# Optimization experiments

Measured on AMD Instinct MI355X. Metric: run time of the kernel, lower is better.

The kernel has to match this reference:

```python
import jax, jax.numpy as jnp
import numpy as np

UNITS = 256
FEAT = 256
NUM_BLOCKS = 4  # start_gru + 2 middle blocks + end_gru
BATCH, T = 128, 384


def _gru_layer(x, kernel, rkernel, bias, return_sequences):
    """Keras GRU (reset_after=True, tanh/sigmoid), zero initial state.
    x: [B,T,D]; kernel: [D,3U]; rkernel: [U,3U]; bias: [2,3U] (input, recurrent).
    Gate order z, r, h as in Keras.
    """
    u = rkernel.shape[0]
    # Precompute input projections for all timesteps (one big GEMM)
    xp = jnp.einsum('btd,dg->btg', x, kernel) + bias[0]  # [B,T,3U]

    def step(h, xt):
        rh = h @ rkernel + bias[1]                 # [B,3U]
        mz, mr, mh = jnp.split(xt, 3, axis=-1)
        rz, rr, rhh = jnp.split(rh, 3, axis=-1)
        z = jax.nn.sigmoid(mz + rz)
        r = jax.nn.sigmoid(mr + rr)
        hh = jnp.tanh(mh + r * rhh)                # reset_after: r applied after recurrent matmul
        h_new = z * h + (1.0 - z) * hh
        return h_new, h_new

    h0 = jnp.zeros((x.shape[0], u), dtype=x.dtype)
    hT, hs = jax.lax.scan(step, h0, jnp.swapaxes(xp, 0, 1))  # scan over time
    return jnp.swapaxes(hs, 0, 1) if return_sequences else hT


def setup_inputs() -> dict:
    key = jax.random.key(0)
    ks = jax.random.split(key, 8)
    s_in = 1.0 / np.sqrt(FEAT)
    s_u = 1.0 / np.sqrt(UNITS)
    x = jax.random.normal(ks[0], (BATCH, T, FEAT), dtype=jnp.float32)
    # first layer params
    k0 = jax.random.normal(ks[1], (FEAT, 3 * UNITS), dtype=jnp.float32) * s_in
    rk0 = jax.random.normal(ks[2], (UNITS, 3 * UNITS), dtype=jnp.float32) * s_u
    b0 = jnp.zeros((2, 3 * UNITS), dtype=jnp.float32)
    # remaining NUM_BLOCKS-1 layers, stacked along leading axis
    L = NUM_BLOCKS - 1
    kern = jax.random.normal(ks[3], (L, UNITS, 3 * UNITS), dtype=jnp.float32) * s_u
    rkern = jax.random.normal(ks[4], (L, UNITS, 3 * UNITS), dtype=jnp.float32) * s_u
    bias = jnp.zeros((L, 2, 3 * UNITS), dtype=jnp.float32)
    return {"x": x, "k0": k0, "rk0": rk0, "b0": b0,
            "kern": kern, "rkern": rkern, "bias": bias}


def reference(x, k0, rk0, b0, kern, rkern, bias):
    # start_gru: return_sequences=True
    h = _gru_layer(x, k0, rk0, b0, return_sequences=True)
    L = kern.shape[0]
    # middle blocks return_sequences=True, last (end_gru) returns final state only
    for i in range(L):
        last = (i == L - 1)
        h = _gru_layer(h, kern[i], rkern[i], bias[i], return_sequences=not last)
    return h  # [B, UNITS]
```

## Files before the change

kernel.cpp:

```cpp
#include <hip/hip_runtime.h>
#include <hip/hip_fp16.h>


#define LAYERS 4
#define TSTEPS 384
#define NCH    8
#define WPL    (48 * 16 * 64 * 8)
#define TILE_STRIDE (16 * 64 * 8)
#define RING   16
#define SLOT_ULL (16 * 128)
#define GRP_ULL  (RING * SLOT_ULL)

typedef _Float16 half8 __attribute__((ext_vector_type(8)));
typedef float    f32x4 __attribute__((ext_vector_type(4)));
typedef unsigned uint4v __attribute__((ext_vector_type(4)));
typedef unsigned long long ull;

#define WP_OFF   0
#define BP_OFF   (LAYERS * WPL * 2)
#define FLAG_OFF (BP_OFF + LAYERS * 1024 * 4)
#define FLAG_BYTES 4096
#define HBUF_OFF (4 * 1024 * 1024)

__global__ void repack_kernel(const float* __restrict__ k0, const float* __restrict__ rk0,
                              const float* __restrict__ b0, const float* __restrict__ kern,
                              const float* __restrict__ rkern, const float* __restrict__ bias,
                              _Float16* __restrict__ Wp, float* __restrict__ Bp)
{
    int idx = blockIdx.x * 256 + threadIdx.x;
    const int total_w = LAYERS * WPL;
    if (idx < total_w) {
        int l = idx / WPL;
        int r = idx - l * WPL;
        int j    = r & 7;
        int lane = (r >> 3) & 63;
        int kt   = (r >> 9) & 15;
        int tile = r >> 13;
        int n = tile * 16 + (lane & 15);
        int k = kt * 32 + (lane >> 4) * 8 + j;
        float v;
        if (l == 0) {
            v = (k < 256) ? k0[(size_t)k * 768 + n] : rk0[(size_t)(k - 256) * 768 + n];
        } else {
            const float* kk = kern  + (size_t)(l - 1) * 256 * 768;
            const float* rk = rkern + (size_t)(l - 1) * 256 * 768;
            v = (k < 256) ? kk[(size_t)k * 768 + n] : rk[(size_t)(k - 256) * 768 + n];
        }
        Wp[idx] = (_Float16)v;
    } else {
        int ib = idx - total_w;
        if (ib < LAYERS * 1024) {
            int l = ib >> 10;
            int i = ib & 1023;
            const float* bs = (l == 0) ? b0 : (bias + (size_t)(l - 1) * 2 * 768);
            float v;
            if (i < 512)      v = bs[i] + bs[768 + i];
            else if (i < 768) v = bs[512 + (i - 512)];
            else              v = bs[768 + 512 + (i - 768)];
            Bp[l * 1024 + i] = v;
        }
    }
}

__launch_bounds__(384, 1)
__global__ void gru_kernel(const float* __restrict__ x,
                           const _Float16* __restrict__ Wp,
                           const float* __restrict__ Bp,
                           ull* __restrict__ hbuf,
                           unsigned int* __restrict__ flags,
                           float* __restrict__ out)
{
    __shared__ _Float16 Af[2][16 * 512];
    __shared__ float    Sc[8][16][17];

    const int tid  = threadIdx.x;
    const int lane = tid & 63;
    const int w    = tid >> 6;
    const int lo16 = lane & 15;
    const int q    = lane >> 4;

    const int s = blockIdx.x & 7;
    const int c = (blockIdx.x >> 3) & 7;
    const int l = blockIdx.x >> 6;
    const int b0row = c * 16;

    const int tile = (w >> 1) * 16 + 2 * s + (w & 1);
    half8 bfrag[16];
    {
        const _Float16* wb = Wp + (size_t)l * WPL + (size_t)tile * TILE_STRIDE;
#pragma unroll
        for (int kt = 0; kt < 16; ++kt)
            bfrag[kt] = *(const half8*)(wb + ((size_t)kt * 64 + lane) * 8);
    }

    const int grow = tid >> 4;
    const int g16  = tid & 15;
    const int gup  = g16 * 2;
    const int ktx  = g16 >> 1;
    const int qq   = (g16 & 1) * 2;
    const int xoff0 = ((ktx * 64) + qq * 16 + grow) * 8;
    const int xoff1 = ((ktx * 64) + (qq + 1) * 16 + grow) * 8;
    const int hoff0 = (((8 + ktx) * 64) + qq * 16 + grow) * 8;
    const int hoff1 = (((8 + ktx) * 64) + (qq + 1) * 16 + grow) * 8;

    float bz[2] = {0,0}, br[2] = {0,0}, bi[2] = {0,0}, bh[2] = {0,0};
    float hprev[2] = {0.f, 0.f};
    if (tid < 256) {
        const float* bp = Bp + l * 1024;
        int ug = s * 32 + gup;
        bz[0] = bp[ug];       bz[1] = bp[ug + 1];
        br[0] = bp[256 + ug]; br[1] = bp[256 + ug + 1];
        bi[0] = bp[512 + ug]; bi[1] = bp[512 + ug + 1];
        bh[0] = bp[768 + ug]; bh[1] = bp[768 + ug + 1];
    }

    unsigned int* fl_own_g = flags + (l * NCH + c) * 16;
    unsigned int* fl_dn_g  = flags + ((l < 3 ? l + 1 : 0) * NCH + c) * 16;
    unsigned int* my_flag  = fl_own_g + s;

    ull*       hb_own = hbuf + (size_t)(l * NCH + c) * GRP_ULL;
    const ull* hb_up  = hbuf + (size_t)((l > 0 ? l - 1 : 0) * NCH + c) * GRP_ULL;

    auto wait_group = [&](const unsigned int* base, unsigned need) {
        for (;;) {
            unsigned v = 0xFFFFFFFFu;
            if (lane < 8)
                v = __hip_atomic_load(base + lane, __ATOMIC_RELAXED,
                                      __HIP_MEMORY_SCOPE_SYSTEM);
            if (__all((int)(v >= need))) return;
            __builtin_amdgcn_s_sleep(1);
        }
    };

    auto stage_x = [&](int t, _Float16* An) {
        if (l == 0) {
            const float* sp = x + ((size_t)(b0row + grow) * TSTEPS + t) * 256 + gup * 8;
            f32x4 a0 = *(const f32x4*)sp,      a1 = *(const f32x4*)(sp + 4);
            f32x4 a2 = *(const f32x4*)(sp + 8), a3 = *(const f32x4*)(sp + 12);
            half8 h0, h1;
            h0[0]=(_Float16)a0[0]; h0[1]=(_Float16)a0[1]; h0[2]=(_Float16)a0[2]; h0[3]=(_Float16)a0[3];
            h0[4]=(_Float16)a1[0]; h0[5]=(_Float16)a1[1]; h0[6]=(_Float16)a1[2]; h0[7]=(_Float16)a1[3];
            h1[0]=(_Float16)a2[0]; h1[1]=(_Float16)a2[1]; h1[2]=(_Float16)a2[2]; h1[3]=(_Float16)a2[3];
            h1[4]=(_Float16)a3[0]; h1[5]=(_Float16)a3[1]; h1[6]=(_Float16)a3[2]; h1[7]=(_Float16)a3[3];
            *(half8*)(An + xoff0) = h0;
            *(half8*)(An + xoff1) = h1;
        } else {
            const ull* spx = hb_up + (size_t)(t & (RING - 1)) * SLOT_ULL + grow * 128 + g16 * 8;
            const unsigned tg = (unsigned)(t + 1);
            ull vx[8];
#pragma unroll
            for (int j = 0; j < 8; ++j)
                vx[j] = __hip_atomic_load(spx + j, __ATOMIC_RELAXED, __HIP_MEMORY_SCOPE_SYSTEM);
            for (;;) {
                bool ok = true;
#pragma unroll
                for (int j = 0; j < 8; ++j)
                    if ((unsigned)(vx[j] >> 32) != tg) {
                        vx[j] = __hip_atomic_load(spx + j, __ATOMIC_RELAXED, __HIP_MEMORY_SCOPE_SYSTEM);
                        ok = false;
                    }
                if (ok) break;
                __builtin_amdgcn_s_sleep(1);
            }
            uint4v w0, w1;
            w0[0]=(unsigned)vx[0]; w0[1]=(unsigned)vx[1]; w0[2]=(unsigned)vx[2]; w0[3]=(unsigned)vx[3];
            w1[0]=(unsigned)vx[4]; w1[1]=(unsigned)vx[5]; w1[2]=(unsigned)vx[6]; w1[3]=(unsigned)vx[7];
            *(uint4v*)(An + xoff0) = w0;
            *(uint4v*)(An + xoff1) = w1;
        }
    };

    if (tid < 256) {
        stage_x(0, Af[0]);
        uint4v z = {0u, 0u, 0u, 0u};
        *(uint4v*)(Af[0] + hoff0) = z;
        *(uint4v*)(Af[0] + hoff1) = z;
    }

    ull vh[8];

    for (int t = 0; t < TSTEPS; ++t) {
        _Float16* A  = Af[t & 1];
        _Float16* An = Af[(t + 1) & 1];

        if (t > 0 && tid < 256) {
            const ull* sph = hb_own + (size_t)((t - 1) & (RING - 1)) * SLOT_ULL + grow * 128 + g16 * 8;
            const unsigned tg = (unsigned)t;
            for (;;) {
                bool ok = true;
#pragma unroll
                for (int j = 0; j < 8; ++j)
                    if ((unsigned)(vh[j] >> 32) != tg) {
                        vh[j] = __hip_atomic_load(sph + j, __ATOMIC_RELAXED, __HIP_MEMORY_SCOPE_SYSTEM);
                        ok = false;
                    }
                if (ok) break;
            }
            uint4v w0, w1;
            w0[0]=(unsigned)vh[0]; w0[1]=(unsigned)vh[1]; w0[2]=(unsigned)vh[2]; w0[3]=(unsigned)vh[3];
            w1[0]=(unsigned)vh[4]; w1[1]=(unsigned)vh[5]; w1[2]=(unsigned)vh[6]; w1[3]=(unsigned)vh[7];
            *(uint4v*)(A + hoff0) = w0;
            *(uint4v*)(A + hoff1) = w1;
        }
        __syncthreads();

        f32x4 acc0 = {0,0,0,0}, acc1 = {0,0,0,0};
#pragma unroll
        for (int kt = 0; kt < 16; ++kt) {
            half8 a = *(const half8*)(A + ((kt * 64) + lane) * 8);
            if (w < 4 || kt < 8)
                acc0 = __builtin_amdgcn_mfma_f32_16x16x32_f16(a, bfrag[kt], acc0, 0, 0, 0);
            else
                acc1 = __builtin_amdgcn_mfma_f32_16x16x32_f16(a, bfrag[kt], acc1, 0, 0, 0);
        }
#pragma unroll
        for (int r = 0; r < 4; ++r) Sc[w][q * 4 + r][lo16] = acc0[r];
        if (w >= 4) {
#pragma unroll
            for (int r = 0; r < 4; ++r) Sc[w + 2][q * 4 + r][lo16] = acc1[r];
        }
        __syncthreads();

        if (l < 3 && t >= RING) wait_group(fl_dn_g, (unsigned)(t - RING + 1));

        if (tid < 256) {
            float hn[2];
#pragma unroll
            for (int j = 0; j < 2; ++j) {
                int u   = gup + j;
                int ut  = u >> 4;
                int col = u & 15;
                float zp = Sc[ut][grow][col]     + bz[j];
                float rp = Sc[2 + ut][grow][col] + br[j];
                float ip = Sc[4 + ut][grow][col] + bi[j];
                float hp = Sc[6 + ut][grow][col] + bh[j];
                float z  = 1.f / (1.f + __expf(-zp));
                float rr = 1.f / (1.f + __expf(-rp));
                float pre = ip + rr * hp;
                float e  = __expf(2.f * pre);
                float th = 1.f - 2.f / (e + 1.f);
                hn[j] = z * hprev[j] + (1.f - z) * th;
                hprev[j] = hn[j];
            }
            union { _Float16 h[2]; unsigned u32; } pk;
            pk.h[0] = (_Float16)hn[0];
            pk.h[1] = (_Float16)hn[1];
            ull word = ((ull)(unsigned)(t + 1) << 32) | (ull)pk.u32;
            __hip_atomic_store(hb_own + (size_t)(t & (RING - 1)) * SLOT_ULL + grow * 128 + s * 16 + g16,
                               word, __ATOMIC_RELAXED, __HIP_MEMORY_SCOPE_SYSTEM);
            if (l == 3 && t == TSTEPS - 1) {
                float* op = out + (size_t)(b0row + grow) * 256 + s * 32 + gup;
                op[0] = hn[0];
                op[1] = hn[1];
            }
        }

        if (t + 1 < TSTEPS && tid < 256) {
            stage_x(t + 1, An);
            const ull* sph = hb_own + (size_t)(t & (RING - 1)) * SLOT_ULL + grow * 128 + g16 * 8;
#pragma unroll
            for (int j = 0; j < 8; ++j)
                vh[j] = __hip_atomic_load(sph + j, __ATOMIC_RELAXED, __HIP_MEMORY_SCOPE_SYSTEM);
        }
        __syncthreads();

        if (tid == 0)
            __hip_atomic_store(my_flag, (unsigned)(t + 1),
                               __ATOMIC_RELAXED, __HIP_MEMORY_SCOPE_SYSTEM);
    }
}

extern "C" void kernel_launch(void* const* d_in, const int* in_sizes, int n_in,
                              void* d_out, int out_size, void* d_ws, size_t ws_size,
                              hipStream_t stream)
{
    const float* x     = (const float*)d_in[0];
    const float* k0    = (const float*)d_in[1];
    const float* rk0   = (const float*)d_in[2];
    const float* b0    = (const float*)d_in[3];
    const float* kern  = (const float*)d_in[4];
    const float* rkern = (const float*)d_in[5];
    const float* bias  = (const float*)d_in[6];
    float* out = (float*)d_out;

    char* ws = (char*)d_ws;
    _Float16*     Wp    = (_Float16*)(ws + WP_OFF);
    float*        Bp    = (float*)(ws + BP_OFF);
    unsigned int* flags = (unsigned int*)(ws + FLAG_OFF);
    ull*          hbuf  = (ull*)(ws + HBUF_OFF);

    hipMemsetAsync(flags, 0, FLAG_BYTES, stream);

    const int total = LAYERS * WPL + LAYERS * 1024;
    repack_kernel<<<(total + 255) / 256, 256, 0, stream>>>(k0, rk0, b0, kern, rkern, bias, Wp, Bp);

    gru_kernel<<<LAYERS * NCH * 8, 384, 0, stream>>>(x, Wp, Bp, hbuf, flags, out);
}
```

Before: 1.714 ms.

## Split GRU into recurrent and input-projection blocks with per-call epoch tags

Moves each layer's input projection out of the recurrent loop and onto separate producer blocks. Two of them per layer and chunk handle alternating timesteps and hand results to the recurrent block through a ring buffer in global memory. Each recurrent block now holds the full 256x768 recurrent weight slice for 16 batch rows in registers and LDS, so the hidden state is exchanged within one workgroup instead of across 8 blocks through global memory. A per-launch epoch counter makes the hbuf tags unique across calls, avoiding stale matches. The cost is more global traffic for the projections, stored as fp16 for z/r, and more complex flag protocols.

```diff
diff --git a/kernel.cpp b/kernel.cpp
--- a/kernel.cpp
+++ b/kernel.cpp
@@ -1,33 +1,41 @@
 #include <hip/hip_runtime.h>
-#include <hip/hip_fp16.h>
 
 
 #define LAYERS 4
 #define TSTEPS 384
-#define NCH    8
-#define WPL    (48 * 16 * 64 * 8)
+#define WPL (48 * 16 * 64 * 8)
 #define TILE_STRIDE (16 * 64 * 8)
-#define RING   16
-#define SLOT_ULL (16 * 128)
-#define GRP_ULL  (RING * SLOT_ULL)
+#define RING_H 16
+#define RING_X 8
+#define HSLOT 2048ull
+#define HGRP (RING_H * HSLOT)
+#define XSLOT_B 32768ull
+#define XGRP_B (RING_X * XSLOT_B)
 
 typedef _Float16 half8 __attribute__((ext_vector_type(8)));
 typedef float    f32x4 __attribute__((ext_vector_type(4)));
-typedef unsigned uint4v __attribute__((ext_vector_type(4)));
 typedef unsigned long long ull;
 
 #define WP_OFF   0
 #define BP_OFF   (LAYERS * WPL * 2)
 #define FLAG_OFF (BP_OFF + LAYERS * 1024 * 4)
 #define FLAG_BYTES 4096
-#define HBUF_OFF (4 * 1024 * 1024)
+#define EP_OFF   (FLAG_OFF + FLAG_BYTES)
+#define HBUF_OFF (4ull << 20)
+#define XP_OFF   (HBUF_OFF + 24ull * HGRP * 8ull)
+
+#define AL __ATOMIC_RELAXED
+#define SS __HIP_MEMORY_SCOPE_SYSTEM
+#define MFMA __builtin_amdgcn_mfma_f32_16x16x32_f16
 
 __global__ void repack_kernel(const float* __restrict__ k0, const float* __restrict__ rk0,
                               const float* __restrict__ b0, const float* __restrict__ kern,
                               const float* __restrict__ rkern, const float* __restrict__ bias,
-                              _Float16* __restrict__ Wp, float* __restrict__ Bp)
+                              _Float16* __restrict__ Wp, float* __restrict__ Bp,
+                              unsigned* __restrict__ ep)
 {
     int idx = blockIdx.x * 256 + threadIdx.x;
+    if (idx == 0) ep[0] = ep[0] + 1u;
     const int total_w = LAYERS * WPL;
     if (idx < total_w) {
         int l = idx / WPL;
@@ -62,211 +70,311 @@
     }
 }
 
-__launch_bounds__(384, 1)
+__launch_bounds__(512, 2)
 __global__ void gru_kernel(const float* __restrict__ x,
                            const _Float16* __restrict__ Wp,
                            const float* __restrict__ Bp,
                            ull* __restrict__ hbuf,
-                           unsigned int* __restrict__ flags,
+                           unsigned* __restrict__ flags,
+                           const unsigned* __restrict__ ep,
+                           char* __restrict__ xpb,
                            float* __restrict__ out)
 {
-    __shared__ _Float16 Af[2][16 * 512];
-    __shared__ float    Sc[8][16][17];
+    __shared__ _Float16 Af[2][8][65][8];
+    __shared__ _Float16 Bl[8][8][64][8];
 
     const int tid  = threadIdx.x;
     const int lane = tid & 63;
     const int w    = tid >> 6;
     const int lo16 = lane & 15;
     const int q    = lane >> 4;
-
-    const int s = blockIdx.x & 7;
-    const int c = (blockIdx.x >> 3) & 7;
-    const int l = blockIdx.x >> 6;
+    const unsigned tagbase = ep[0] * 1024u;
+
+    const bool isrec = (blockIdx.x < 32);
+    int l, c, par = 0;
+    if (isrec) { l = blockIdx.x >> 3; c = blockIdx.x & 7; }
+    else { int p = blockIdx.x - 32; l = p >> 4; c = (p >> 1) & 7; par = p & 1; }
     const int b0row = c * 16;
 
-    const int tile = (w >> 1) * 16 + 2 * s + (w & 1);
-    half8 bfrag[16];
+    half8 bf0[8], bf1[8], bf2[8], bf3[8], bf4[8];
     {
-        const _Float16* wb = Wp + (size_t)l * WPL + (size_t)tile * TILE_STRIDE;
-#pragma unroll
-        for (int kt = 0; kt < 16; ++kt)
-            bfrag[kt] = *(const half8*)(wb + ((size_t)kt * 64 + lane) * 8);
+        const _Float16* wb = Wp + (size_t)l * WPL;
+        const int kb = isrec ? 8 : 0;
+        const int t0 = 2*w, t1 = 2*w+1, t2 = 16+2*w, t3 = 17+2*w, t4 = 32+2*w, t5 = 33+2*w;
+#pragma unroll
+        for (int kt = 0; kt < 8; ++kt) {
+            size_t o = (size_t)((kb + kt) * 64 + lane) * 8;
+            bf0[kt] = *(const half8*)(wb + (size_t)t0 * TILE_STRIDE + o);
+            bf1[kt] = *(const half8*)(wb + (size_t)t1 * TILE_STRIDE + o);
+            bf2[kt] = *(const half8*)(wb + (size_t)t2 * TILE_STRIDE + o);
+            bf3[kt] = *(const half8*)(wb + (size_t)t3 * TILE_STRIDE + o);
+            bf4[kt] = *(const half8*)(wb + (size_t)t4 * TILE_STRIDE + o);
+            *(half8*)&Bl[w][kt][lane][0] = *(const half8*)(wb + (size_t)t5 * TILE_STRIDE + o);
+        }
     }
 
-    const int grow = tid >> 4;
-    const int g16  = tid & 15;
-    const int gup  = g16 * 2;
-    const int ktx  = g16 >> 1;
-    const int qq   = (g16 & 1) * 2;
-    const int xoff0 = ((ktx * 64) + qq * 16 + grow) * 8;
-    const int xoff1 = ((ktx * 64) + (qq + 1) * 16 + grow) * 8;
-    const int hoff0 = (((8 + ktx) * 64) + qq * 16 + grow) * 8;
-    const int hoff1 = (((8 + ktx) * 64) + (qq + 1) * 16 + grow) * 8;
-
-    float bz[2] = {0,0}, br[2] = {0,0}, bi[2] = {0,0}, bh[2] = {0,0};
-    float hprev[2] = {0.f, 0.f};
-    if (tid < 256) {
-        const float* bp = Bp + l * 1024;
-        int ug = s * 32 + gup;
-        bz[0] = bp[ug];       bz[1] = bp[ug + 1];
-        br[0] = bp[256 + ug]; br[1] = bp[256 + ug + 1];
-        bi[0] = bp[512 + ug]; bi[1] = bp[512 + ug + 1];
-        bh[0] = bp[768 + ug]; bh[1] = bp[768 + ug + 1];
-    }
-
-    unsigned int* fl_own_g = flags + (l * NCH + c) * 16;
-    unsigned int* fl_dn_g  = flags + ((l < 3 ? l + 1 : 0) * NCH + c) * 16;
-    unsigned int* my_flag  = fl_own_g + s;
-
-    ull*       hb_own = hbuf + (size_t)(l * NCH + c) * GRP_ULL;
-    const ull* hb_up  = hbuf + (size_t)((l > 0 ? l - 1 : 0) * NCH + c) * GRP_ULL;
-
-    auto wait_group = [&](const unsigned int* base, unsigned need) {
-        for (;;) {
-            unsigned v = 0xFFFFFFFFu;
-            if (lane < 8)
-                v = __hip_atomic_load(base + lane, __ATOMIC_RELAXED,
-                                      __HIP_MEMORY_SCOPE_SYSTEM);
-            if (__all((int)(v >= need))) return;
+    if (isrec) {
+        ull* hb_own = hbuf + (size_t)(l * 8 + c) * HGRP;
+        char* xg = xpb + (size_t)(l * 8 + c) * XGRP_B;
+        unsigned* rprog = flags + 128 + (l * 8 + c);
+        const ull* xf_pair = (const ull*)(flags + (l * 8 + c) * 2);
+        const ull* pp_pair = (const ull*)(flags + ((l < 3 ? l + 1 : l) * 8 + c) * 2);
+
+        float bh0, bh1;
+        {
+            const float* bp = Bp + l * 1024;
+            bh0 = bp[768 + 32 * w + lo16];
+            bh1 = bp[768 + 32 * w + 16 + lo16];
+        }
+
+        if (tid < 520) {
+            half8 z8 = {};
+            *(half8*)&Af[0][tid / 65][tid % 65][0] = z8;
+        }
+
+        float hprev[2][4] = {{0,0,0,0},{0,0,0,0}};
+        ull xzr[4], xip[4];
+        ull xfv, ppv = 0;
+
+        xfv = __hip_atomic_load(xf_pair, AL, SS);
+        while ((unsigned)(xfv & 0xffffffffu) < 1u) {
             __builtin_amdgcn_s_sleep(1);
-        }
-    };
-
-    auto stage_x = [&](int t, _Float16* An) {
-        if (l == 0) {
-            const float* sp = x + ((size_t)(b0row + grow) * TSTEPS + t) * 256 + gup * 8;
-            f32x4 a0 = *(const f32x4*)sp,      a1 = *(const f32x4*)(sp + 4);
-            f32x4 a2 = *(const f32x4*)(sp + 8), a3 = *(const f32x4*)(sp + 12);
-            half8 h0, h1;
-            h0[0]=(_Float16)a0[0]; h0[1]=(_Float16)a0[1]; h0[2]=(_Float16)a0[2]; h0[3]=(_Float16)a0[3];
-            h0[4]=(_Float16)a1[0]; h0[5]=(_Float16)a1[1]; h0[6]=(_Float16)a1[2]; h0[7]=(_Float16)a1[3];
-            h1[0]=(_Float16)a2[0]; h1[1]=(_Float16)a2[1]; h1[2]=(_Float16)a2[2]; h1[3]=(_Float16)a2[3];
-            h1[4]=(_Float16)a3[0]; h1[5]=(_Float16)a3[1]; h1[6]=(_Float16)a3[2]; h1[7]=(_Float16)a3[3];
-            *(half8*)(An + xoff0) = h0;
-            *(half8*)(An + xoff1) = h1;
-        } else {
-            const ull* spx = hb_up + (size_t)(t & (RING - 1)) * SLOT_ULL + grow * 128 + g16 * 8;
-            const unsigned tg = (unsigned)(t + 1);
-            ull vx[8];
-#pragma unroll
-            for (int j = 0; j < 8; ++j)
-                vx[j] = __hip_atomic_load(spx + j, __ATOMIC_RELAXED, __HIP_MEMORY_SCOPE_SYSTEM);
-            for (;;) {
-                bool ok = true;
-#pragma unroll
-                for (int j = 0; j < 8; ++j)
-                    if ((unsigned)(vx[j] >> 32) != tg) {
-                        vx[j] = __hip_atomic_load(spx + j, __ATOMIC_RELAXED, __HIP_MEMORY_SCOPE_SYSTEM);
-                        ok = false;
+            xfv = __hip_atomic_load(xf_pair, AL, SS);
+        }
+        {
+            const ull* xz = (const ull*)xg;
+            const ull* xi = (const ull*)(xg + 16384);
+#pragma unroll
+            for (int g = 0; g < 4; ++g)
+                xzr[g] = __hip_atomic_load(xz + (w * 4 + g) * 64 + lane, AL, SS);
+#pragma unroll
+            for (int gi = 0; gi < 2; ++gi)
+#pragma unroll
+                for (int h2 = 0; h2 < 2; ++h2)
+                    xip[gi * 2 + h2] = __hip_atomic_load(xi + ((w * 2 + gi) * 64 + lane) * 2 + h2, AL, SS);
+        }
+        xfv = __hip_atomic_load(xf_pair, AL, SS);
+        if (l < 3) ppv = __hip_atomic_load(pp_pair, AL, SS);
+        __syncthreads();
+
+        for (int t = 0; t < TSTEPS; ++t) {
+            const int cb = t & 1, nb = cb ^ 1;
+
+            f32x4 acc0, acc1, acc2, acc3, acc4, acc5;
+            {
+                union { ull u; _Float16 h[4]; } v0, v1, v2, v3;
+                v0.u = xzr[0]; v1.u = xzr[1]; v2.u = xzr[2]; v3.u = xzr[3];
+                acc0 = (f32x4){(float)v0.h[0], (float)v0.h[1], (float)v0.h[2], (float)v0.h[3]};
+                acc1 = (f32x4){(float)v1.h[0], (float)v1.h[1], (float)v1.h[2], (float)v1.h[3]};
+                acc2 = (f32x4){(float)v2.h[0], (float)v2.h[1], (float)v2.h[2], (float)v2.h[3]};
+                acc3 = (f32x4){(float)v3.h[0], (float)v3.h[1], (float)v3.h[2], (float)v3.h[3]};
+            }
+            acc4 = (f32x4){bh0, bh0, bh0, bh0};
+            acc5 = (f32x4){bh1, bh1, bh1, bh1};
+
+#pragma unroll
+            for (int kt = 0; kt < 8; ++kt) {
+                half8 a  = *(const half8*)&Af[cb][kt][lane][0];
+                half8 bl = *(const half8*)&Bl[w][kt][lane][0];
+                acc0 = MFMA(a, bf0[kt], acc0, 0, 0, 0);
+                acc1 = MFMA(a, bf1[kt], acc1, 0, 0, 0);
+                acc2 = MFMA(a, bf2[kt], acc2, 0, 0, 0);
+                acc3 = MFMA(a, bf3[kt], acc3, 0, 0, 0);
+                acc4 = MFMA(a, bf4[kt], acc4, 0, 0, 0);
+                acc5 = MFMA(a, bl,      acc5, 0, 0, 0);
+            }
+
+            float hn[2][4];
+            {
+                union { ull u; float f[2]; } i0, i1, i2, i3;
+                i0.u = xip[0]; i1.u = xip[1]; i2.u = xip[2]; i3.u = xip[3];
+                const float ipv[2][4] = {{i0.f[0], i0.f[1], i1.f[0], i1.f[1]},
+                                         {i2.f[0], i2.f[1], i3.f[0], i3.f[1]}};
+#pragma unroll
+                for (int uu = 0; uu < 2; ++uu) {
+#pragma unroll
+                    for (int j = 0; j < 4; ++j) {
+                        float zp = uu ? acc1[j] : acc0[j];
+                        float rp = uu ? acc3[j] : acc2[j];
+                        float hp = uu ? acc5[j] : acc4[j];
+                        float z  = 1.f / (1.f + __expf(-zp));
+                        float r  = 1.f / (1.f + __expf(-rp));
+                        float pre = ipv[uu][j] + r * hp;
+                        float e  = __expf(2.f * pre);
+                        float th = 1.f - 2.f / (e + 1.f);
+                        float h  = z * hprev[uu][j] + (1.f - z) * th;
+                        hprev[uu][j] = h;
+                        hn[uu][j] = h;
                     }
-                if (ok) break;
-                __builtin_amdgcn_s_sleep(1);
-            }
-            uint4v w0, w1;
-            w0[0]=(unsigned)vx[0]; w0[1]=(unsigned)vx[1]; w0[2]=(unsigned)vx[2]; w0[3]=(unsigned)vx[3];
-            w1[0]=(unsigned)vx[4]; w1[1]=(unsigned)vx[5]; w1[2]=(unsigned)vx[6]; w1[3]=(unsigned)vx[7];
-            *(uint4v*)(An + xoff0) = w0;
-            *(uint4v*)(An + xoff1) = w1;
-        }
-    };
-
-    if (tid < 256) {
-        stage_x(0, Af[0]);
-        uint4v z = {0u, 0u, 0u, 0u};
-        *(uint4v*)(Af[0] + hoff0) = z;
-        *(uint4v*)(Af[0] + hoff1) = z;
-    }
-
-    ull vh[8];
-
-    for (int t = 0; t < TSTEPS; ++t) {
-        _Float16* A  = Af[t & 1];
-        _Float16* An = Af[(t + 1) & 1];
-
-        if (t > 0 && tid < 256) {
-            const ull* sph = hb_own + (size_t)((t - 1) & (RING - 1)) * SLOT_ULL + grow * 128 + g16 * 8;
-            const unsigned tg = (unsigned)t;
-            for (;;) {
-                bool ok = true;
-#pragma unroll
-                for (int j = 0; j < 8; ++j)
-                    if ((unsigned)(vh[j] >> 32) != tg) {
-                        vh[j] = __hip_atomic_load(sph + j, __ATOMIC_RELAXED, __HIP_MEMORY_SCOPE_SYSTEM);
-                        ok = false;
+                }
+            }
+
+#pragma unroll
+            for (int uu = 0; uu < 2; ++uu) {
+                const int lg = 2 * uu + (lo16 >> 3);
+                const int j7 = lo16 & 7;
+#pragma unroll
+                for (int j = 0; j < 4; ++j)
+                    Af[nb][w][lg * 16 + q * 4 + j][j7] = (_Float16)hn[uu][j];
+            }
+            if (l == 3 && t == TSTEPS - 1) {
+#pragma unroll
+                for (int uu = 0; uu < 2; ++uu)
+#pragma unroll
+                    for (int j = 0; j < 4; ++j)
+                        out[(size_t)(b0row + q * 4 + j) * 256 + 32 * w + uu * 16 + lo16] = hn[uu][j];
+            }
+            __syncthreads();
+
+            if (t + 1 < TSTEPS) {
+                const unsigned need = (unsigned)(t + 2);
+                unsigned fv = (unsigned)(((t + 1) & 1) ? (xfv >> 32) : (xfv & 0xffffffffu));
+                while (fv < need) {
+                    __builtin_amdgcn_s_sleep(1);
+                    xfv = __hip_atomic_load(xf_pair, AL, SS);
+                    fv = (unsigned)(((t + 1) & 1) ? (xfv >> 32) : (xfv & 0xffffffffu));
+                }
+                const char* xs = xg + (size_t)((t + 1) & (RING_X - 1)) * XSLOT_B;
+                const ull* xz = (const ull*)xs;
+                const ull* xi = (const ull*)(xs + 16384);
+#pragma unroll
+                for (int g = 0; g < 4; ++g)
+                    xzr[g] = __hip_atomic_load(xz + (w * 4 + g) * 64 + lane, AL, SS);
+#pragma unroll
+                for (int gi = 0; gi < 2; ++gi)
+#pragma unroll
+                    for (int h2 = 0; h2 < 2; ++h2)
+                        xip[gi * 2 + h2] = __hip_atomic_load(xi + ((w * 2 + gi) * 64 + lane) * 2 + h2, AL, SS);
+            }
+            if (l < 3) {
+                if (t >= RING_H) {
+                    const unsigned need = (unsigned)(t - RING_H + 1);
+                    unsigned p0 = (unsigned)(ppv & 0xffffffffu), p1 = (unsigned)(ppv >> 32);
+                    while (p0 < need || p1 < need) {
+                        __builtin_amdgcn_s_sleep(1);
+                        ppv = __hip_atomic_load(pp_pair, AL, SS);
+                        p0 = (unsigned)(ppv & 0xffffffffu); p1 = (unsigned)(ppv >> 32);
                     }
-                if (ok) break;
-            }
-            uint4v w0, w1;
-            w0[0]=(unsigned)vh[0]; w0[1]=(unsigned)vh[1]; w0[2]=(unsigned)vh[2]; w0[3]=(unsigned)vh[3];
-            w1[0]=(unsigned)vh[4]; w1[1]=(unsigned)vh[5]; w1[2]=(unsigned)vh[6]; w1[3]=(unsigned)vh[7];
-            *(uint4v*)(A + hoff0) = w0;
-            *(uint4v*)(A + hoff1) = w1;
-        }
-        __syncthreads();
-
-        f32x4 acc0 = {0,0,0,0}, acc1 = {0,0,0,0};
-#pragma unroll
-        for (int kt = 0; kt < 16; ++kt) {
-            half8 a = *(const half8*)(A + ((kt * 64) + lane) * 8);
-            if (w < 4 || kt < 8)
-                acc0 = __builtin_amdgcn_mfma_f32_16x16x32_f16(a, bfrag[kt], acc0, 0, 0, 0);
-            else
-                acc1 = __builtin_amdgcn_mfma_f32_16x16x32_f16(a, bfrag[kt], acc1, 0, 0, 0);
-        }
-#pragma unroll
-        for (int r = 0; r < 4; ++r) Sc[w][q * 4 + r][lo16] = acc0[r];
-        if (w >= 4) {
-#pragma unroll
-            for (int r = 0; r < 4; ++r) Sc[w + 2][q * 4 + r][lo16] = acc1[r];
-        }
-        __syncthreads();
-
-        if (l < 3 && t >= RING) wait_group(fl_dn_g, (unsigned)(t - RING + 1));
-
-        if (tid < 256) {
-            float hn[2];
-#pragma unroll
-            for (int j = 0; j < 2; ++j) {
-                int u   = gup + j;
-                int ut  = u >> 4;
-                int col = u & 15;
-                float zp = Sc[ut][grow][col]     + bz[j];
-                float rp = Sc[2 + ut][grow][col] + br[j];
-                float ip = Sc[4 + ut][grow][col] + bi[j];
-                float hp = Sc[6 + ut][grow][col] + bh[j];
-                float z  = 1.f / (1.f + __expf(-zp));
-                float rr = 1.f / (1.f + __expf(-rp));
-                float pre = ip + rr * hp;
-                float e  = __expf(2.f * pre);
-                float th = 1.f - 2.f / (e + 1.f);
-                hn[j] = z * hprev[j] + (1.f - z) * th;
-                hprev[j] = hn[j];
-            }
-            union { _Float16 h[2]; unsigned u32; } pk;
-            pk.h[0] = (_Float16)hn[0];
-            pk.h[1] = (_Float16)hn[1];
-            ull word = ((ull)(unsigned)(t + 1) << 32) | (ull)pk.u32;
-            __hip_atomic_store(hb_own + (size_t)(t & (RING - 1)) * SLOT_ULL + grow * 128 + s * 16 + g16,
-                               word, __ATOMIC_RELAXED, __HIP_MEMORY_SCOPE_SYSTEM);
-            if (l == 3 && t == TSTEPS - 1) {
-                float* op = out + (size_t)(b0row + grow) * 256 + s * 32 + gup;
-                op[0] = hn[0];
-                op[1] = hn[1];
-            }
-        }
-
-        if (t + 1 < TSTEPS && tid < 256) {
-            stage_x(t + 1, An);
-            const ull* sph = hb_own + (size_t)(t & (RING - 1)) * SLOT_ULL + grow * 128 + g16 * 8;
-#pragma unroll
-            for (int j = 0; j < 8; ++j)
-                vh[j] = __hip_atomic_load(sph + j, __ATOMIC_RELAXED, __HIP_MEMORY_SCOPE_SYSTEM);
-        }
-        __syncthreads();
-
-        if (tid == 0)
-            __hip_atomic_store(my_flag, (unsigned)(t + 1),
-                               __ATOMIC_RELAXED, __HIP_MEMORY_SCOPE_SYSTEM);
+                }
+                const int row = tid >> 5, wq = tid & 31;
+                ull* dst = hb_own + (size_t)(t & (RING_H - 1)) * HSLOT + row * 128 + wq * 4;
+                const ull tg = ((ull)(tagbase + (unsigned)(t + 1))) << 32;
+#pragma unroll
+                for (int m = 0; m < 4; ++m) {
+                    const int wi = wq * 4 + m;
+                    const unsigned v = *(const unsigned*)&Af[nb][wi >> 4][((wi >> 2) & 3) * 16 + row][(wi & 3) * 2];
+                    __hip_atomic_store(dst + m, tg | (ull)v, AL, SS);
+                }
+                ppv = __hip_atomic_load(pp_pair, AL, SS);
+            }
+            if (t + 1 < TSTEPS) xfv = __hip_atomic_load(xf_pair, AL, SS);
+            if (tid == 0) __hip_atomic_store(rprog, (unsigned)(t + 1), AL, SS);
+        }
+    } else {
+        const ull* hb_up = hbuf + (size_t)((l > 0 ? l - 1 : 0) * 8 + c) * HGRP;
+        char* xg = xpb + (size_t)(l * 8 + c) * XGRP_B;
+        unsigned* my_flag = flags + (l * 8 + c) * 2 + par;
+        unsigned* rprog = flags + 128 + (l * 8 + c);
+        float bz0, bz1, br0, br1, bi0, bi1;
+        {
+            const float* bp = Bp + l * 1024;
+            const int u0 = 32 * w + lo16, u1 = u0 + 16;
+            bz0 = bp[u0];       bz1 = bp[u1];
+            br0 = bp[256 + u0]; br1 = bp[256 + u1];
+            bi0 = bp[512 + u0]; bi1 = bp[512 + u1];
+        }
+        unsigned rpv = 0;
+        const int row = tid >> 5, g16x = tid & 31;
+
+        for (int t = par; t < TSTEPS; t += 2) {
+            if (l == 0) {
+                const float* sp = x + ((size_t)(b0row + row) * TSTEPS + t) * 256 + g16x * 8;
+                f32x4 a0 = *(const f32x4*)sp;
+                f32x4 a1 = *(const f32x4*)(sp + 4);
+                half8 hh;
+                hh[0] = (_Float16)a0[0]; hh[1] = (_Float16)a0[1];
+                hh[2] = (_Float16)a0[2]; hh[3] = (_Float16)a0[3];
+                hh[4] = (_Float16)a1[0]; hh[5] = (_Float16)a1[1];
+                hh[6] = (_Float16)a1[2]; hh[7] = (_Float16)a1[3];
+                *(half8*)&Af[0][g16x >> 2][(g16x & 3) * 16 + row][0] = hh;
+            } else {
+                const ull* spx = hb_up + (size_t)(t & (RING_H - 1)) * HSLOT + row * 128 + g16x * 4;
+                const unsigned tg = tagbase + (unsigned)(t + 1);
+                ull v0 = __hip_atomic_load(spx + 0, AL, SS);
+                ull v1 = __hip_atomic_load(spx + 1, AL, SS);
+                ull v2 = __hip_atomic_load(spx + 2, AL, SS);
+                ull v3 = __hip_atomic_load(spx + 3, AL, SS);
+                for (;;) {
+                    bool ok = true;
+                    if ((unsigned)(v0 >> 32) != tg) { v0 = __hip_atomic_load(spx + 0, AL, SS); ok = false; }
+                    if ((unsigned)(v1 >> 32) != tg) { v1 = __hip_atomic_load(spx + 1, AL, SS); ok = false; }
+                    if ((unsigned)(v2 >> 32) != tg) { v2 = __hip_atomic_load(spx + 2, AL, SS); ok = false; }
+                    if ((unsigned)(v3 >> 32) != tg) { v3 = __hip_atomic_load(spx + 3, AL, SS); ok = false; }
+                    if (ok) break;
+                    __builtin_amdgcn_s_sleep(1);
+                }
+                union { unsigned u[4]; half8 h; } pk;
+                pk.u[0] = (unsigned)v0; pk.u[1] = (unsigned)v1;
+                pk.u[2] = (unsigned)v2; pk.u[3] = (unsigned)v3;
+                *(half8*)&Af[0][g16x >> 2][(g16x & 3) * 16 + row][0] = pk.h;
+            }
+            __syncthreads();
+
+            f32x4 acc0 = {bz0, bz0, bz0, bz0}, acc1 = {bz1, bz1, bz1, bz1};
+            f32x4 acc2 = {br0, br0, br0, br0}, acc3 = {br1, br1, br1, br1};
+            f32x4 acc4 = {bi0, bi0, bi0, bi0}, acc5 = {bi1, bi1, bi1, bi1};
+#pragma unroll
+            for (int kt = 0; kt < 8; ++kt) {
+                half8 a  = *(const half8*)&Af[0][kt][lane][0];
+                half8 bl = *(const half8*)&Bl[w][kt][lane][0];
+                acc0 = MFMA(a, bf0[kt], acc0, 0, 0, 0);
+                acc1 = MFMA(a, bf1[kt], acc1, 0, 0, 0);
+                acc2 = MFMA(a, bf2[kt], acc2, 0, 0, 0);
+                acc3 = MFMA(a, bf3[kt], acc3, 0, 0, 0);
+                acc4 = MFMA(a, bf4[kt], acc4, 0, 0, 0);
+                acc5 = MFMA(a, bl,      acc5, 0, 0, 0);
+            }
+            __syncthreads();
+
+            if (t >= RING_X) {
+                const unsigned need = (unsigned)(t - RING_X + 1);
+                while (rpv < need) {
+                    __builtin_amdgcn_s_sleep(1);
+                    rpv = __hip_atomic_load(rprog, AL, SS);
+                }
+            }
+
+            {
+                char* xs = xg + (size_t)(t & (RING_X - 1)) * XSLOT_B;
+                ull* xz = (ull*)xs;
+                ull* xi = (ull*)(xs + 16384);
+                union { ull u; _Float16 h[4]; } pz;
+                pz.h[0] = (_Float16)acc0[0]; pz.h[1] = (_Float16)acc0[1];
+                pz.h[2] = (_Float16)acc0[2]; pz.h[3] = (_Float16)acc0[3];
+                __hip_atomic_store(xz + (w * 4 + 0) * 64 + lane, pz.u, AL, SS);
+                pz.h[0] = (_Float16)acc1[0]; pz.h[1] = (_Float16)acc1[1];
+                pz.h[2] = (_Float16)acc1[2]; pz.h[3] = (_Float16)acc1[3];
+                __hip_atomic_store(xz + (w * 4 + 1) * 64 + lane, pz.u, AL, SS);
+                pz.h[0] = (_Float16)acc2[0]; pz.h[1] = (_Float16)acc2[1];
+                pz.h[2] = (_Float16)acc2[2]; pz.h[3] = (_Float16)acc2[3];
+                __hip_atomic_store(xz + (w * 4 + 2) * 64 + lane, pz.u, AL, SS);
+                pz.h[0] = (_Float16)acc3[0]; pz.h[1] = (_Float16)acc3[1];
+                pz.h[2] = (_Float16)acc3[2]; pz.h[3] = (_Float16)acc3[3];
+                __hip_atomic_store(xz + (w * 4 + 3) * 64 + lane, pz.u, AL, SS);
+                union { ull u; float f[2]; } pi;
+                pi.f[0] = acc4[0]; pi.f[1] = acc4[1];
+                __hip_atomic_store(xi + ((w * 2 + 0) * 64 + lane) * 2 + 0, pi.u, AL, SS);
+                pi.f[0] = acc4[2]; pi.f[1] = acc4[3];
+                __hip_atomic_store(xi + ((w * 2 + 0) * 64 + lane) * 2 + 1, pi.u, AL, SS);
+                pi.f[0] = acc5[0]; pi.f[1] = acc5[1];
+                __hip_atomic_store(xi + ((w * 2 + 1) * 64 + lane) * 2 + 0, pi.u, AL, SS);
+                pi.f[0] = acc5[2]; pi.f[1] = acc5[3];
+                __hip_atomic_store(xi + ((w * 2 + 1) * 64 + lane) * 2 + 1, pi.u, AL, SS);
+            }
+            __syncthreads();
+            if (tid == 0) __hip_atomic_store(my_flag, (unsigned)(t + 1), AL, SS);
+            rpv = __hip_atomic_load(rprog, AL, SS);
+        }
     }
 }
 
@@ -284,15 +392,17 @@
     float* out = (float*)d_out;
 
     char* ws = (char*)d_ws;
-    _Float16*     Wp    = (_Float16*)(ws + WP_OFF);
-    float*        Bp    = (float*)(ws + BP_OFF);
-    unsigned int* flags = (unsigned int*)(ws + FLAG_OFF);
-    ull*          hbuf  = (ull*)(ws + HBUF_OFF);
+    _Float16*  Wp    = (_Float16*)(ws + WP_OFF);
+    float*     Bp    = (float*)(ws + BP_OFF);
+    unsigned*  flags = (unsigned*)(ws + FLAG_OFF);
+    unsigned*  ep    = (unsigned*)(ws + EP_OFF);
+    ull*       hbuf  = (ull*)(ws + HBUF_OFF);
+    char*      xpb   = ws + XP_OFF;
 
     hipMemsetAsync(flags, 0, FLAG_BYTES, stream);
 
     const int total = LAYERS * WPL + LAYERS * 1024;
-    repack_kernel<<<(total + 255) / 256, 256, 0, stream>>>(k0, rk0, b0, kern, rkern, bias, Wp, Bp);
-
-    gru_kernel<<<LAYERS * NCH * 8, 384, 0, stream>>>(x, Wp, Bp, hbuf, flags, out);
+    repack_kernel<<<(total + 255) / 256, 256, 0, stream>>>(k0, rk0, b0, kern, rkern, bias, Wp, Bp, ep);
+
+    gru_kernel<<<96, 512, 0, stream>>>(x, Wp, Bp, hbuf, flags, ep, xpb, out);
 }
```

Result: slower. 2.228 ms (+30.0%).
